# Performance work log

Hardware: AMD Instinct MI355X
Metric: run time of the kernel (lower is better)

## Reference

```python
import jax, jax.numpy as jnp
import numpy as np

N = 100000
E = 1600000
CIN = 32
COUT = 32
K = 5
EPS = 1e-15      # PyG GMMConv EPS in sigma^2 denominator
BN_EPS = 1e-5    # torch BatchNorm1d default eps


def gmm_conv(x, edge_index, edge_attr, g, mu, sigma, root, bias):
    """PyG GMMConv (MoNet), aggr='mean', root_weight=True, bias=True."""
    src, dst = edge_index[0], edge_index[1]
    n = x.shape[0]
    k = mu.shape[0]
    cout = root.shape[1]
    xg = (x @ g).reshape(n, k, cout)                # [N, K, out]
    xj = xg[src]                                    # gather: [E, K, out]
    d = edge_attr[:, None, :] - mu[None, :, :]      # [E, K, 3]
    w = jnp.exp(-0.5 * jnp.sum(d * d / (EPS + sigma[None] ** 2), axis=-1))  # [E, K]
    msg = jnp.einsum('eko,ek->eo', xj, w)           # [E, out]
    agg = jax.ops.segment_sum(msg, dst, num_segments=n)
    cnt = jax.ops.segment_sum(jnp.ones((msg.shape[0],), x.dtype), dst, num_segments=n)
    agg = agg / jnp.clip(cnt, 1.0)[:, None]         # mean aggregation
    return agg + x @ root + bias


def batch_norm(x, gamma, beta):
    # training-mode BatchNorm1d: biased batch statistics over node dim
    m = x.mean(0)
    v = x.var(0)
    return (x - m) * jax.lax.rsqrt(v + BN_EPS) * gamma + beta


def setup_inputs() -> dict:
    key = jax.random.key(0)
    ks = jax.random.split(key, 12)
    p = lambda k, s, sc=0.1: jax.random.normal(k, s, jnp.float32) * sc
    return {
        'x': jax.random.normal(ks[0], (N, CIN), jnp.float32),
        'edge_index': jax.random.randint(ks[1], (2, E), 0, N, jnp.int32),
        'edge_attr': jax.random.uniform(ks[2], (E, 3), jnp.float32),
        # left conv1: in -> out, K=5
        'g1': p(ks[3], (CIN, K * COUT)), 'mu1': p(ks[4], (K, 3), 1.0), 'sigma1': jnp.ones((K, 3), jnp.float32),
        'root1': p(ks[5], (CIN, COUT)), 'b1': jnp.zeros((COUT,), jnp.float32),
        'gam1': jnp.ones((COUT,), jnp.float32), 'bet1': jnp.zeros((COUT,), jnp.float32),
        # left conv2: out -> out, K=5
        'g2': p(ks[6], (COUT, K * COUT)), 'mu2': p(ks[7], (K, 3), 1.0), 'sigma2': jnp.ones((K, 3), jnp.float32),
        'root2': p(ks[8], (COUT, COUT)), 'b2': jnp.zeros((COUT,), jnp.float32),
        'gam2': jnp.ones((COUT,), jnp.float32), 'bet2': jnp.zeros((COUT,), jnp.float32),
        # shortcut conv: in -> out, K=1
        'gs': p(ks[9], (CIN, 1 * COUT)), 'mus': p(ks[10], (1, 3), 1.0), 'sigmas': jnp.ones((1, 3), jnp.float32),
        'roots': p(ks[11], (CIN, COUT)), 'bs': jnp.zeros((COUT,), jnp.float32),
        'gams': jnp.ones((COUT,), jnp.float32), 'bets': jnp.zeros((COUT,), jnp.float32),
    }


def reference(x, edge_index, edge_attr,
              g1, mu1, sigma1, root1, b1, gam1, bet1,
              g2, mu2, sigma2, root2, b2, gam2, bet2,
              gs, mus, sigmas, roots, bs, gams, bets):
    h = jax.nn.elu(batch_norm(gmm_conv(x, edge_index, edge_attr, g1, mu1, sigma1, root1, b1), gam1, bet1))
    h = batch_norm(gmm_conv(h, edge_index, edge_attr, g2, mu2, sigma2, root2, b2), gam2, bet2)
    s = batch_norm(gmm_conv(x, edge_index, edge_attr, gs, mus, sigmas, roots, bs), gams, bets)
    return jax.nn.elu(h + s)
```

## Files before the change

kernel.cpp:

```cpp
#include <hip/hip_runtime.h>
#include <hip/hip_bf16.h>
#include <math.h>


#define ELU(v) ((v) > 0.f ? (v) : (__expf(v) - 1.f))

using short8  = __attribute__((ext_vector_type(8))) short;
using floatx4 = __attribute__((ext_vector_type(4))) float;
using uintx4  = __attribute__((ext_vector_type(4))) unsigned;

__device__ inline ushort f2bf(float f) {
    __hip_bfloat16 h = __float2bfloat16(f);
    return *reinterpret_cast<ushort*>(&h);
}
__device__ inline float bflo(unsigned u) { return __uint_as_float(u << 16); }
__device__ inline float bfhi(unsigned u) { return __uint_as_float(u & 0xffff0000u); }
__device__ inline unsigned pack_bf2(float lo, float hi) {
    return ((unsigned)f2bf(hi) << 16) | (unsigned)f2bf(lo);
}

__global__ __launch_bounds__(256) void prep_xb(
    const float* __restrict__ x, unsigned* __restrict__ XB, int N)
{
    const int idx = blockIdx.x * blockDim.x + threadIdx.x;
    if (idx >= N * 16) return;
    const float2 p = ((const float2*)x)[idx];
    XB[idx] = pack_bf2(p.x, p.y);
}

__global__ __launch_bounds__(256) void prep_hxb(
    const float* __restrict__ out1, const float* __restrict__ coef,
    unsigned* __restrict__ XB, int N)
{
    const int idx = blockIdx.x * blockDim.x + threadIdx.x;
    if (idx >= N * 16) return;
    const int l = idx & 15;
    const float2 p = ((const float2*)out1)[idx];
    const int c0 = 2 * l, c1 = 2 * l + 1;
    float v0 = p.x * coef[c0] + coef[32 + c0];
    float v1 = p.y * coef[c1] + coef[32 + c1];
    v0 = ELU(v0); v1 = ELU(v1);
    XB[idx] = pack_bf2(v0, v1);
}

__global__ __launch_bounds__(256) void packb_k(
    const float* __restrict__ g1, const float* __restrict__ root1,
    const float* __restrict__ gs, const float* __restrict__ roots,
    const float* __restrict__ g2, const float* __restrict__ root2,
    uintx4* __restrict__ PA, uintx4* __restrict__ PB)
{
    const int idx = blockIdx.x * 256 + threadIdx.x;
    if (idx >= 1536) return;
    const int lane = idx & 63;
    const int s = (idx >> 6) % 6;
    const int wv = idx / (6 * 64);
    const int l4 = lane & 15, quad = lane >> 4, half = wv & 1;

    auto pack = [&](const float* src, int ld, int col) {
        ushort u[8];
#pragma unroll
        for (int j = 0; j < 8; ++j) u[j] = f2bf(src[(quad * 8 + j) * ld + col]);
        uintx4 v;
        v.x = (unsigned)u[0] | ((unsigned)u[1] << 16);
        v.y = (unsigned)u[2] | ((unsigned)u[3] << 16);
        v.z = (unsigned)u[4] | ((unsigned)u[5] << 16);
        v.w = (unsigned)u[6] | ((unsigned)u[7] << 16);
        return v;
    };

    {
        uintx4 v = {0u, 0u, 0u, 0u};
        if (wv < 2) {
            if (s < 5) v = pack(g1, 160, s * 32 + 16 * half + l4);
            else       v = pack(root1, 32, 16 * half + l4);
        } else {
            if (s == 0)      v = pack(gs, 32, 16 * half + l4);
            else if (s == 1) v = pack(roots, 32, 16 * half + l4);
        }
        PA[idx] = v;
    }
    if (wv < 2) {
        uintx4 v;
        if (s < 5) v = pack(g2, 160, s * 32 + 16 * half + l4);
        else       v = pack(root2, 32, 16 * half + l4);
        PB[idx] = v;
    }
}

#define CH 4096
__global__ __launch_bounds__(256) void binfill_k(
    const int* __restrict__ ei, const float* __restrict__ attr,
    int* __restrict__ gcur, unsigned long long* __restrict__ pay0,
    int E, int NB, int CAPc)
{
    __shared__ unsigned long long srec[CH];
    __shared__ unsigned char sbin[CH];
    __shared__ int cnt[256], offs[256], wcur[256], gbase[256], sc[256];

    const int t = threadIdx.x;
    const int e0 = blockIdx.x * CH;
    const int nrec = min(CH, E - e0);

    cnt[t] = 0;
    __syncthreads();

    unsigned long long rec[16];
    int bin[16];
#pragma unroll
    for (int r = 0; r < 16; ++r) {
        const int e = e0 + r * 256 + t;
        bin[r] = -1;
        if (e < E) {
            const int s = ei[e], d = ei[E + e];
            const float a0 = attr[(size_t)e * 3 + 0];
            const float a1 = attr[(size_t)e * 3 + 1];
            const float a2 = attr[(size_t)e * 3 + 2];
            const unsigned q0 = (unsigned)min(max((int)(a0 * 4096.f), 0), 4095);
            const unsigned q1 = (unsigned)min(max((int)(a1 * 4096.f), 0), 4095);
            const unsigned q2 = (unsigned)min(max((int)(a2 * 4096.f), 0), 4095);
            rec[r] = (unsigned long long)(unsigned)s
                   | ((unsigned long long)(d & 511) << 17)
                   | ((unsigned long long)q0 << 26)
                   | ((unsigned long long)q1 << 38)
                   | ((unsigned long long)q2 << 50);
            bin[r] = d >> 9;
            atomicAdd(&cnt[bin[r]], 1);
        }
    }
    __syncthreads();

    const int v = cnt[t];
    sc[t] = v;
    __syncthreads();
    for (int o = 1; o < 256; o <<= 1) {
        const int xx = (t >= o) ? sc[t - o] : 0;
        __syncthreads();
        sc[t] += xx;
        __syncthreads();
    }
    offs[t] = sc[t] - v;
    wcur[t] = sc[t] - v;
    __syncthreads();

#pragma unroll
    for (int r = 0; r < 16; ++r) {
        if (bin[r] >= 0) {
            const int pos = atomicAdd(&wcur[bin[r]], 1);
            srec[pos] = rec[r];
            sbin[pos] = (unsigned char)bin[r];
        }
    }
    __syncthreads();

    if (t < NB && cnt[t] > 0) gbase[t] = atomicAdd(&gcur[t], cnt[t]);
    __syncthreads();

    for (int i = t; i < nrec; i += 256) {
        const int b = sbin[i];
        const int idx = gbase[b] + (i - offs[b]);
        if (idx < CAPc)
            pay0[(size_t)b * CAPc + idx] = srec[i];
    }
}

__global__ __launch_bounds__(256) void scatter2_k(
    const unsigned long long* __restrict__ pay0, const int* __restrict__ gcur,
    int* __restrict__ row_ptr, unsigned long long* __restrict__ pay,
    int N, int CAPc, int NB)
{
    const int b = blockIdx.x;
    const int t = threadIdx.x;
    const int d0 = b << 9;
    const int nd = min(512, N - d0);

    __shared__ int cnt[512];
    __shared__ int offs[512];
    __shared__ int sscan[256];
    __shared__ int ssum[256];

    ssum[t] = (t < b && t < NB) ? gcur[t] : 0;
    for (int i = t; i < 512; i += 256) cnt[i] = 0;
    __syncthreads();
    for (int o = 128; o > 0; o >>= 1) {
        if (t < o) ssum[t] += ssum[t + o];
        __syncthreads();
    }
    const int base = ssum[0];

    const int total = min(gcur[b], CAPc);
    const unsigned long long* src = pay0 + (size_t)b * CAPc;

    for (int i = t; i < total; i += 256) {
        const int dlo = (int)((src[i] >> 17) & 511);
        atomicAdd(&cnt[dlo], 1);
    }
    __syncthreads();

    const int c0 = cnt[2 * t], c1 = cnt[2 * t + 1];
    const int pairsum = c0 + c1;
    sscan[t] = pairsum;
    __syncthreads();
    for (int o = 1; o < 256; o <<= 1) {
        const int xx = (t >= o) ? sscan[t - o] : 0;
        __syncthreads();
        sscan[t] += xx;
        __syncthreads();
    }
    const int excl = sscan[t] - pairsum;
    offs[2 * t] = excl;
    offs[2 * t + 1] = excl + c0;
    __syncthreads();
    const int btotal = sscan[255];

    for (int i = t; i < nd; i += 256) row_ptr[d0 + i] = base + offs[i];
    if (b == NB - 1 && t == 0) row_ptr[N] = base + btotal;

    for (int i = t; i < 512; i += 256) cnt[i] = offs[i];
    __syncthreads();

    for (int i = t; i < total; i += 256) {
        const unsigned long long rec = src[i];
        const int dlo = (int)((rec >> 17) & 511);
        const int p = atomicAdd(&cnt[dlo], 1);
        pay[base + p] = rec;
    }
}

template <bool HAS_S>
__global__ __launch_bounds__(256, 8) void gt_k(
    const unsigned* __restrict__ XB,
    const unsigned long long* __restrict__ payload,
    const int* __restrict__ row_ptr,
    const float* __restrict__ mu_m, const float* __restrict__ sg_m,
    const float* __restrict__ mu_s, const float* __restrict__ sg_s,
    const uintx4* __restrict__ PBT,
    const float* __restrict__ bm,
    const float* __restrict__ bss,
    float* __restrict__ out_m, float* __restrict__ out_s,
    float* __restrict__ stats_m, float* __restrict__ stats_s,
    int N, int ntiles)
{
    constexpr int KS = HAS_S ? 6 : 5;
    constexpr int SLS = KS + 1;
    constexpr int STRIDE = SLS * 16 + 4;
    constexpr float DQ = 1.0f / 4096.0f;

    __shared__ float wbuf[16][17][8];
    __shared__ unsigned sA[16 * STRIDE];
    __shared__ float sred[128];

    const int tid = threadIdx.x;
    const int l = tid & 15, grp = tid >> 4;
    const int lane = tid & 63, l4 = lane & 15, quad = lane >> 4;
    const int wv = tid >> 6;
    const int half = wv & 1;

    const bool convRole = (wv < 2);
    const bool sRole = HAS_S && (wv >= 2);
    float bias0 = 0.f;
    if (convRole)      bias0 = bm[16 * half + l4];
    else if (sRole)    bias0 = bss[16 * half + l4];

    float mm[15], im[15];
#pragma unroll
    for (int i = 0; i < 15; ++i) {
        mm[i] = mu_m[i];
        float s = sg_m[i];
        im[i] = 1.0f / (1e-15f + s * s);
    }
    float ms[3], is[3];
    if (HAS_S) {
#pragma unroll
        for (int i = 0; i < 3; ++i) {
            ms[i] = mu_s[i];
            float s = sg_s[i];
            is[i] = 1.0f / (1e-15f + s * s);
        }
    }

    float ps = 0.f, pq = 0.f;

    for (int tile = blockIdx.x; tile < ntiles; tile += gridDim.x) {
        const int dst = tile * 16 + grp;
        float2 acc[KS];
#pragma unroll
        for (int k = 0; k < KS; ++k) acc[k] = make_float2(0.f, 0.f);

        int rp0 = 0, deg = 0;
        if (dst < N) { rp0 = row_ptr[dst]; deg = row_ptr[dst + 1] - rp0; }

        auto body = [&](int j) {
            const float4 a = *(const float4*)&wbuf[grp][j][0];
            const float4 b = *(const float4*)&wbuf[grp][j][4];
            const int sj = __float_as_int(a.x);
            const unsigned u = XB[(size_t)sj * 16 + l];
            const float x0 = bflo(u), x1 = bfhi(u);
            acc[0].x = fmaf(a.y, x0, acc[0].x); acc[0].y = fmaf(a.y, x1, acc[0].y);
            acc[1].x = fmaf(a.z, x0, acc[1].x); acc[1].y = fmaf(a.z, x1, acc[1].y);
            acc[2].x = fmaf(a.w, x0, acc[2].x); acc[2].y = fmaf(a.w, x1, acc[2].y);
            acc[3].x = fmaf(b.x, x0, acc[3].x); acc[3].y = fmaf(b.x, x1, acc[3].y);
            acc[4].x = fmaf(b.y, x0, acc[4].x); acc[4].y = fmaf(b.y, x1, acc[4].y);
            if (HAS_S) {
                acc[5].x = fmaf(b.z, x0, acc[5].x); acc[5].y = fmaf(b.z, x1, acc[5].y);
            }
        };

        for (int base = 0; base < deg; base += 16) {
            const int nj = min(16, deg - base);
            if (l < nj) {
                unsigned long long pq8 = payload[rp0 + base + l];
                const int src = (int)(pq8 & 0x1FFFFull);
                float p0 = ((int)((pq8 >> 26) & 0xFFF) + 0.5f) * DQ;
                float p1 = ((int)((pq8 >> 38) & 0xFFF) + 0.5f) * DQ;
                float p2 = ((int)((pq8 >> 50) & 0xFFF) + 0.5f) * DQ;
                float w[5], wS = 0.f;
#pragma unroll
                for (int k = 0; k < 5; ++k) {
                    float d0 = p0 - mm[k * 3 + 0];
                    float d1 = p1 - mm[k * 3 + 1];
                    float d2 = p2 - mm[k * 3 + 2];
                    float q = d0 * d0 * im[k * 3 + 0] + d1 * d1 * im[k * 3 + 1]
                            + d2 * d2 * im[k * 3 + 2];
                    w[k] = __expf(-0.5f * q);
                }
                if (HAS_S) {
                    float d0 = p0 - ms[0], d1 = p1 - ms[1], d2 = p2 - ms[2];
                    float q = d0 * d0 * is[0] + d1 * d1 * is[1] + d2 * d2 * is[2];
                    wS = __expf(-0.5f * q);
                }
                float4* wp = (float4*)&wbuf[grp][l][0];
                wp[0] = make_float4(__int_as_float(src), w[0], w[1], w[2]);
                wp[1] = make_float4(w[3], w[4], wS, 0.f);
            }
            int j = 0;
            for (; j + 3 < nj; j += 4) { body(j); body(j + 1); body(j + 2); body(j + 3); }
            for (; j < nj; ++j) body(j);
        }

        {
            unsigned* arow = sA + grp * STRIDE;
            const float invd = 1.0f / fmaxf((float)deg, 1.0f);
            const bool ok = (dst < N);
#pragma unroll
            for (int k = 0; k < KS; ++k)
                arow[k * 16 + l] = ok ? pack_bf2(acc[k].x * invd, acc[k].y * invd) : 0u;
            arow[KS * 16 + l] = ok ? XB[(size_t)dst * 16 + l] : 0u;
        }
        __syncthreads();

        if (convRole || sRole) {
            floatx4 C = {0.f, 0.f, 0.f, 0.f};
            if (convRole) {
                uintx4 bv[6];
#pragma unroll
                for (int s = 0; s < 6; ++s)
                    bv[s] = *(const volatile uintx4*)(PBT + (wv * 6 + s) * 64 + lane);
#pragma unroll
                for (int s = 0; s < 6; ++s) {
                    const int slot = (s < 5) ? s : KS;
                    const uint4 av = *(const uint4*)(sA + l4 * STRIDE + slot * 16 + quad * 4);
                    const short8 A = *reinterpret_cast<const short8*>(&av);
                    const short8 B = *reinterpret_cast<const short8*>(&bv[s]);
                    C = __builtin_amdgcn_mfma_f32_16x16x32_bf16(A, B, C, 0, 0, 0);
                }
            } else {
                uintx4 bv[2];
#pragma unroll
                for (int s = 0; s < 2; ++s)
                    bv[s] = *(const volatile uintx4*)(PBT + (wv * 6 + s) * 64 + lane);
#pragma unroll
                for (int s = 0; s < 2; ++s) {
                    const int slot = 5 + s;
                    const uint4 av = *(const uint4*)(sA + l4 * STRIDE + slot * 16 + quad * 4);
                    const short8 A = *reinterpret_cast<const short8*>(&av);
                    const short8 B = *reinterpret_cast<const short8*>(&bv[s]);
                    C = __builtin_amdgcn_mfma_f32_16x16x32_bf16(A, B, C, 0, 0, 0);
                }
            }

            float* outp = convRole ? out_m : out_s;
#pragma unroll
            for (int r = 0; r < 4; ++r) {
                const int n = tile * 16 + quad * 4 + r;
                if (n < N) {
                    const float v = C[r] + bias0;
                    outp[(size_t)n * 32 + 16 * half + l4] = v;
                    ps += v; pq += v * v;
                }
            }
        }
        __syncthreads();
    }

    if (tid < 128) sred[tid] = 0.f;
    __syncthreads();
    if (convRole) {
        atomicAdd(&sred[16 * half + l4], ps);
        atomicAdd(&sred[32 + 16 * half + l4], pq);
    } else if (sRole) {
        atomicAdd(&sred[64 + 16 * half + l4], ps);
        atomicAdd(&sred[96 + 16 * half + l4], pq);
    }
    __syncthreads();
    const int spread = (blockIdx.x & 7) * 64;
    if (tid < 64) atomicAdd(&stats_m[spread + tid], sred[tid]);
    else if (HAS_S && tid < 128) atomicAdd(&stats_s[spread + tid - 64], sred[tid]);
}

__global__ void coef2_k(const float* __restrict__ stats1, const float* __restrict__ gam1,
                        const float* __restrict__ bet1, float* __restrict__ coef1,
                        const float* __restrict__ stats2, const float* __restrict__ gam2,
                        const float* __restrict__ bet2, float* __restrict__ coef2,
                        float invN)
{
    const int t = threadIdx.x;
    const int set = t >> 6;
    const int c = t & 63;
    if (c >= 32) return;
    const float* stats = set ? stats2 : stats1;
    const float* gam = set ? gam2 : gam1;
    const float* bet = set ? bet2 : bet1;
    float* coef = set ? coef2 : coef1;
    if (set && !stats) return;
    float s = 0.f, q = 0.f;
    for (int p = 0; p < 8; ++p) { s += stats[p * 64 + c]; q += stats[p * 64 + 32 + c]; }
    float m = s * invN;
    float v = fmaxf(q * invN - m * m, 0.f);
    float sc = gam[c] * rsqrtf(v + 1e-5f);
    coef[c] = sc;
    coef[32 + c] = bet[c] - m * sc;
}

__global__ __launch_bounds__(256) void final_k(
    const float* __restrict__ o2, const float* __restrict__ os,
    const float* __restrict__ c2, const float* __restrict__ cs,
    float* __restrict__ out, int total)
{
    int idx = blockIdx.x * blockDim.x + threadIdx.x;
    if (idx >= total) return;
    int c = idx & 31;
    float v = o2[idx] * c2[c] + c2[32 + c] + os[idx] * cs[c] + cs[32 + c];
    out[idx] = ELU(v);
}

extern "C" void kernel_launch(void* const* d_in, const int* in_sizes, int n_in,
                              void* d_out, int out_size, void* d_ws, size_t ws_size,
                              hipStream_t stream)
{
    const float* x      = (const float*)d_in[0];
    const int*   ei     = (const int*)d_in[1];
    const float* attr   = (const float*)d_in[2];
    const float* g1     = (const float*)d_in[3];
    const float* mu1    = (const float*)d_in[4];
    const float* sig1   = (const float*)d_in[5];
    const float* root1  = (const float*)d_in[6];
    const float* b1     = (const float*)d_in[7];
    const float* gam1   = (const float*)d_in[8];
    const float* bet1   = (const float*)d_in[9];
    const float* g2     = (const float*)d_in[10];
    const float* mu2    = (const float*)d_in[11];
    const float* sig2   = (const float*)d_in[12];
    const float* root2  = (const float*)d_in[13];
    const float* b2     = (const float*)d_in[14];
    const float* gam2   = (const float*)d_in[15];
    const float* bet2   = (const float*)d_in[16];
    const float* gs     = (const float*)d_in[17];
    const float* mus    = (const float*)d_in[18];
    const float* sigs   = (const float*)d_in[19];
    const float* roots  = (const float*)d_in[20];
    const float* bs     = (const float*)d_in[21];
    const float* gams   = (const float*)d_in[22];
    const float* bets   = (const float*)d_in[23];

    const int N = in_sizes[0] / 32;
    const int E = in_sizes[1] / 2;
    const int total = N * 32;
    const int ntiles = (N + 15) / 16;
    const int NB = (N + 511) >> 9;
    const int CAPc = ((((E + NB - 1) / NB) * 5) / 4 + 15) & ~15;

    char* ws = (char*)d_ws;
    size_t off = 0;
    auto carve = [&](size_t bytes) {
        void* p = ws + off;
        off = (off + bytes + 255) & ~(size_t)255;
        return p;
    };
    unsigned* XB   = (unsigned*)carve((size_t)N * 16 * 4);
    float*  OUT1   = (float*)carve((size_t)N * 32 * 4);
    float*  OUT2   = (float*)carve((size_t)N * 32 * 4);
    float*  OUTS   = (float*)carve((size_t)N * 32 * 4);
    unsigned long long* PAY  = (unsigned long long*)carve((size_t)E * 8);
    unsigned long long* PAY0 = (unsigned long long*)carve((size_t)NB * CAPc * 8);
    int*    ROWP   = (int*)carve((size_t)(N + 1) * 4);
    int*    GCUR   = (int*)carve(256 * 4);
    float*  STATS  = (float*)carve(3 * 512 * 4);
    float*  COEF   = (float*)carve(3 * 64 * 4);
    uintx4* PBA    = (uintx4*)carve(1536 * 16);
    uintx4* PBB    = (uintx4*)carve(1536 * 16);
    float* stats1 = STATS, *stats2 = STATS + 512, *statsS = STATS + 1024;
    float* coef1 = COEF, *coef2 = COEF + 64, *coefS = COEF + 128;
    (void)ws_size; (void)n_in; (void)out_size;

    const float invN = 1.0f / (float)N;
    const int ew = (total + 255) / 256;
    const int epb = (N * 16 + 255) / 256;
    const int nfb = (E + CH - 1) / CH;
    const int gtb = ntiles < 2048 ? ntiles : 2048;

    hipMemsetAsync(GCUR, 0, 256 * 4, stream);
    hipMemsetAsync(STATS, 0, 3 * 512 * 4, stream);

    binfill_k<<<nfb, 256, 0, stream>>>(ei, attr, GCUR, PAY0, E, NB, CAPc);
    packb_k<<<6, 256, 0, stream>>>(g1, root1, gs, roots, g2, root2, PBA, PBB);
    scatter2_k<<<NB, 256, 0, stream>>>(PAY0, GCUR, ROWP, PAY, N, CAPc, NB);

    prep_xb<<<epb, 256, 0, stream>>>(x, XB, N);
    gt_k<true><<<gtb, 256, 0, stream>>>(XB, PAY, ROWP,
        mu1, sig1, mus, sigs, PBA, b1, bs,
        OUT1, OUTS, stats1, statsS, N, ntiles);
    coef2_k<<<1, 128, 0, stream>>>(stats1, gam1, bet1, coef1,
                                   statsS, gams, bets, coefS, invN);

    prep_hxb<<<epb, 256, 0, stream>>>(OUT1, coef1, XB, N);
    gt_k<false><<<gtb, 256, 0, stream>>>(XB, PAY, ROWP,
        mu2, sig2, nullptr, nullptr, PBB, b2, nullptr,
        OUT2, nullptr, stats2, nullptr, N, ntiles);
    coef2_k<<<1, 128, 0, stream>>>(stats2, gam2, bet2, coef2,
                                   nullptr, nullptr, nullptr, nullptr, invN);

    final_k<<<ew, 256, 0, stream>>>(OUT2, OUTS, coef2, coefS, (float*)d_out, total);
}
```

Before: 376.8 us.

## Precompute Gaussian edge weights in scatter and store fp16 payloads per layer

The Gaussian mixture weights for both conv layers and the shortcut are now computed once per edge in the CSR scatter kernel and stored as fp16 pairs in two 16-byte payload arrays. The gather kernels no longer unpack quantised coordinates or evaluate exps per edge. This moves exp work out of the latency-bound gather loop. In exchange, payload traffic per edge grows from 8 to 16 bytes per layer, extra writes are added in scatter, and the weights lose some precision in fp16. The MFMA B-operand loads are also split into two groups of three, which lowers register pressure.

Result: faster. 336.8 us (-10.6%).

```diff
diff --git a/kernel.cpp b/kernel.cpp
--- a/kernel.cpp
+++ b/kernel.cpp
@@ -1,5 +1,6 @@
 #include <hip/hip_runtime.h>
 #include <hip/hip_bf16.h>
+#include <hip/hip_fp16.h>
 #include <math.h>
 
 
@@ -17,6 +18,14 @@
 __device__ inline float bfhi(unsigned u) { return __uint_as_float(u & 0xffff0000u); }
 __device__ inline unsigned pack_bf2(float lo, float hi) {
     return ((unsigned)f2bf(hi) << 16) | (unsigned)f2bf(lo);
+}
+__device__ inline unsigned pack_h2(float lo, float hi) {
+    __half2 h = __floats2half2_rn(lo, hi);
+    return *reinterpret_cast<unsigned*>(&h);
+}
+__device__ inline float2 unpack_h2(unsigned u) {
+    __half2 h = *reinterpret_cast<__half2*>(&u);
+    return __half22float2(h);
 }
 
 __global__ __launch_bounds__(256) void prep_xb(
@@ -165,9 +174,14 @@
 
 __global__ __launch_bounds__(256) void scatter2_k(
     const unsigned long long* __restrict__ pay0, const int* __restrict__ gcur,
-    int* __restrict__ row_ptr, unsigned long long* __restrict__ pay,
+    int* __restrict__ row_ptr,
+    uint4* __restrict__ payA, uint4* __restrict__ payB,
+    const float* __restrict__ mu1, const float* __restrict__ sg1,
+    const float* __restrict__ mus, const float* __restrict__ sgs,
+    const float* __restrict__ mu2, const float* __restrict__ sg2,
     int N, int CAPc, int NB)
 {
+    constexpr float DQ = 1.0f / 4096.0f;
     const int b = blockIdx.x;
     const int t = threadIdx.x;
     const int d0 = b << 9;
@@ -178,6 +192,17 @@
     __shared__ int sscan[256];
     __shared__ int ssum[256];
 
+    float m1[15], i1[15], m2[15], i2[15], msv[3], isv[3];
+#pragma unroll
+    for (int i = 0; i < 15; ++i) {
+        m1[i] = mu1[i];  { float s = sg1[i]; i1[i] = 1.0f / (1e-15f + s * s); }
+        m2[i] = mu2[i];  { float s = sg2[i]; i2[i] = 1.0f / (1e-15f + s * s); }
+    }
+#pragma unroll
+    for (int i = 0; i < 3; ++i) {
+        msv[i] = mus[i]; { float s = sgs[i]; isv[i] = 1.0f / (1e-15f + s * s); }
+    }
+
     ssum[t] = (t < b && t < NB) ? gcur[t] : 0;
     for (int i = t; i < 512; i += 256) cnt[i] = 0;
     __syncthreads();
@@ -222,17 +247,48 @@
         const unsigned long long rec = src[i];
         const int dlo = (int)((rec >> 17) & 511);
         const int p = atomicAdd(&cnt[dlo], 1);
-        pay[base + p] = rec;
+        const unsigned srcn = (unsigned)(rec & 0x1FFFFull);
+        const float p0 = ((int)((rec >> 26) & 0xFFF) + 0.5f) * DQ;
+        const float p1 = ((int)((rec >> 38) & 0xFFF) + 0.5f) * DQ;
+        const float p2 = ((int)((rec >> 50) & 0xFFF) + 0.5f) * DQ;
+        float w1[5], w2[5];
+#pragma unroll
+        for (int k = 0; k < 5; ++k) {
+            {
+                const float d0 = p0 - m1[k * 3 + 0];
+                const float d1 = p1 - m1[k * 3 + 1];
+                const float d2 = p2 - m1[k * 3 + 2];
+                const float q = d0 * d0 * i1[k * 3 + 0] + d1 * d1 * i1[k * 3 + 1]
+                              + d2 * d2 * i1[k * 3 + 2];
+                w1[k] = __expf(-0.5f * q);
+            }
+            {
+                const float d0 = p0 - m2[k * 3 + 0];
+                const float d1 = p1 - m2[k * 3 + 1];
+                const float d2 = p2 - m2[k * 3 + 2];
+                const float q = d0 * d0 * i2[k * 3 + 0] + d1 * d1 * i2[k * 3 + 1]
+                              + d2 * d2 * i2[k * 3 + 2];
+                w2[k] = __expf(-0.5f * q);
+            }
+        }
+        float wS;
+        {
+            const float d0 = p0 - msv[0], d1 = p1 - msv[1], d2 = p2 - msv[2];
+            const float q = d0 * d0 * isv[0] + d1 * d1 * isv[1] + d2 * d2 * isv[2];
+            wS = __expf(-0.5f * q);
+        }
+        payA[base + p] = make_uint4(srcn, pack_h2(w1[0], w1[1]),
+                                    pack_h2(w1[2], w1[3]), pack_h2(w1[4], wS));
+        payB[base + p] = make_uint4(srcn, pack_h2(w2[0], w2[1]),
+                                    pack_h2(w2[2], w2[3]), pack_h2(w2[4], 0.f));
     }
 }
 
 template <bool HAS_S>
 __global__ __launch_bounds__(256, 8) void gt_k(
     const unsigned* __restrict__ XB,
-    const unsigned long long* __restrict__ payload,
+    const uint4* __restrict__ payload,
     const int* __restrict__ row_ptr,
-    const float* __restrict__ mu_m, const float* __restrict__ sg_m,
-    const float* __restrict__ mu_s, const float* __restrict__ sg_s,
     const uintx4* __restrict__ PBT,
     const float* __restrict__ bm,
     const float* __restrict__ bss,
@@ -243,7 +299,6 @@
     constexpr int KS = HAS_S ? 6 : 5;
     constexpr int SLS = KS + 1;
     constexpr int STRIDE = SLS * 16 + 4;
-    constexpr float DQ = 1.0f / 4096.0f;
 
     __shared__ float wbuf[16][17][8];
     __shared__ unsigned sA[16 * STRIDE];
@@ -260,23 +315,6 @@
     float bias0 = 0.f;
     if (convRole)      bias0 = bm[16 * half + l4];
     else if (sRole)    bias0 = bss[16 * half + l4];
-
-    float mm[15], im[15];
-#pragma unroll
-    for (int i = 0; i < 15; ++i) {
-        mm[i] = mu_m[i];
-        float s = sg_m[i];
-        im[i] = 1.0f / (1e-15f + s * s);
-    }
-    float ms[3], is[3];
-    if (HAS_S) {
-#pragma unroll
-        for (int i = 0; i < 3; ++i) {
-            ms[i] = mu_s[i];
-            float s = sg_s[i];
-            is[i] = 1.0f / (1e-15f + s * s);
-        }
-    }
 
     float ps = 0.f, pq = 0.f;
 
@@ -308,29 +346,13 @@
         for (int base = 0; base < deg; base += 16) {
             const int nj = min(16, deg - base);
             if (l < nj) {
-                unsigned long long pq8 = payload[rp0 + base + l];
-                const int src = (int)(pq8 & 0x1FFFFull);
-                float p0 = ((int)((pq8 >> 26) & 0xFFF) + 0.5f) * DQ;
-                float p1 = ((int)((pq8 >> 38) & 0xFFF) + 0.5f) * DQ;
-                float p2 = ((int)((pq8 >> 50) & 0xFFF) + 0.5f) * DQ;
-                float w[5], wS = 0.f;
-#pragma unroll
-                for (int k = 0; k < 5; ++k) {
-                    float d0 = p0 - mm[k * 3 + 0];
-                    float d1 = p1 - mm[k * 3 + 1];
-                    float d2 = p2 - mm[k * 3 + 2];
-                    float q = d0 * d0 * im[k * 3 + 0] + d1 * d1 * im[k * 3 + 1]
-                            + d2 * d2 * im[k * 3 + 2];
-                    w[k] = __expf(-0.5f * q);
-                }
-                if (HAS_S) {
-                    float d0 = p0 - ms[0], d1 = p1 - ms[1], d2 = p2 - ms[2];
-                    float q = d0 * d0 * is[0] + d1 * d1 * is[1] + d2 * d2 * is[2];
-                    wS = __expf(-0.5f * q);
-                }
+                const uint4 rec = payload[rp0 + base + l];
+                const float2 w01 = unpack_h2(rec.y);
+                const float2 w23 = unpack_h2(rec.z);
+                const float2 w4S = unpack_h2(rec.w);
                 float4* wp = (float4*)&wbuf[grp][l][0];
-                wp[0] = make_float4(__int_as_float(src), w[0], w[1], w[2]);
-                wp[1] = make_float4(w[3], w[4], wS, 0.f);
+                wp[0] = make_float4(__uint_as_float(rec.x), w01.x, w01.y, w23.x);
+                wp[1] = make_float4(w23.y, w4S.x, w4S.y, 0.f);
             }
             int j = 0;
             for (; j + 3 < nj; j += 4) { body(j); body(j + 1); body(j + 2); body(j + 3); }
@@ -351,17 +373,21 @@
         if (convRole || sRole) {
             floatx4 C = {0.f, 0.f, 0.f, 0.f};
             if (convRole) {
-                uintx4 bv[6];
-#pragma unroll
-                for (int s = 0; s < 6; ++s)
-                    bv[s] = *(const volatile uintx4*)(PBT + (wv * 6 + s) * 64 + lane);
-#pragma unroll
-                for (int s = 0; s < 6; ++s) {
-                    const int slot = (s < 5) ? s : KS;
-                    const uint4 av = *(const uint4*)(sA + l4 * STRIDE + slot * 16 + quad * 4);
-                    const short8 A = *reinterpret_cast<const short8*>(&av);
-                    const short8 B = *reinterpret_cast<const short8*>(&bv[s]);
-                    C = __builtin_amdgcn_mfma_f32_16x16x32_bf16(A, B, C, 0, 0, 0);
+#pragma unroll
+                for (int g3 = 0; g3 < 2; ++g3) {
+                    uintx4 bv[3];
+#pragma unroll
+                    for (int s = 0; s < 3; ++s)
+                        bv[s] = *(const volatile uintx4*)(PBT + (wv * 6 + g3 * 3 + s) * 64 + lane);
+#pragma unroll
+                    for (int s = 0; s < 3; ++s) {
+                        const int ss = g3 * 3 + s;
+                        const int slot = (ss < 5) ? ss : KS;
+                        const uint4 av = *(const uint4*)(sA + l4 * STRIDE + slot * 16 + quad * 4);
+                        const short8 A = *reinterpret_cast<const short8*>(&av);
+                        const short8 B = *reinterpret_cast<const short8*>(&bv[s]);
+                        C = __builtin_amdgcn_mfma_f32_16x16x32_bf16(A, B, C, 0, 0, 0);
+                    }
                 }
             } else {
                 uintx4 bv[2];
@@ -490,7 +516,8 @@
     float*  OUT1   = (float*)carve((size_t)N * 32 * 4);
     float*  OUT2   = (float*)carve((size_t)N * 32 * 4);
     float*  OUTS   = (float*)carve((size_t)N * 32 * 4);
-    unsigned long long* PAY  = (unsigned long long*)carve((size_t)E * 8);
+    uint4*  PAYA   = (uint4*)carve((size_t)E * 16);
+    uint4*  PAYB   = (uint4*)carve((size_t)E * 16);
     unsigned long long* PAY0 = (unsigned long long*)carve((size_t)NB * CAPc * 8);
     int*    ROWP   = (int*)carve((size_t)(N + 1) * 4);
     int*    GCUR   = (int*)carve(256 * 4);
@@ -513,19 +540,19 @@
 
     binfill_k<<<nfb, 256, 0, stream>>>(ei, attr, GCUR, PAY0, E, NB, CAPc);
     packb_k<<<6, 256, 0, stream>>>(g1, root1, gs, roots, g2, root2, PBA, PBB);
-    scatter2_k<<<NB, 256, 0, stream>>>(PAY0, GCUR, ROWP, PAY, N, CAPc, NB);
+    scatter2_k<<<NB, 256, 0, stream>>>(PAY0, GCUR, ROWP, PAYA, PAYB,
+                                       mu1, sig1, mus, sigs, mu2, sig2,
+                                       N, CAPc, NB);
 
     prep_xb<<<epb, 256, 0, stream>>>(x, XB, N);
-    gt_k<true><<<gtb, 256, 0, stream>>>(XB, PAY, ROWP,
-        mu1, sig1, mus, sigs, PBA, b1, bs,
-        OUT1, OUTS, stats1, statsS, N, ntiles);
+    gt_k<true><<<gtb, 256, 0, stream>>>(XB, PAYA, ROWP,
+        PBA, b1, bs, OUT1, OUTS, stats1, statsS, N, ntiles);
     coef2_k<<<1, 128, 0, stream>>>(stats1, gam1, bet1, coef1,
                                    statsS, gams, bets, coefS, invN);
 
     prep_hxb<<<epb, 256, 0, stream>>>(OUT1, coef1, XB, N);
-    gt_k<false><<<gtb, 256, 0, stream>>>(XB, PAY, ROWP,
-        mu2, sig2, nullptr, nullptr, PBB, b2, nullptr,
-        OUT2, nullptr, stats2, nullptr, N, ntiles);
+    gt_k<false><<<gtb, 256, 0, stream>>>(XB, PAYB, ROWP,
+        PBB, b2, nullptr, OUT2, nullptr, stats2, nullptr, N, ntiles);
     coef2_k<<<1, 128, 0, stream>>>(stats2, gam2, bet2, coef2,
                                    nullptr, nullptr, nullptr, nullptr, invN);
 
```
